# Kernel tuning notes

Hardware: AMD Instinct MI355X
Metric: run time of the kernel (lower is better)

Reference implementation:

```python
import jax, jax.numpy as jnp
import numpy as np

N = 50000


def gcn_conv(x, W, b, src, dst, deg_inv_sqrt):
    # h = x @ W, then symmetric-normalized aggregation with self-loops
    h = x @ W  # [N, out]
    norm = deg_inv_sqrt[src] * deg_inv_sqrt[dst]  # [E]
    agg = jax.ops.segment_sum(h[src] * norm[:, None], dst, num_segments=N)
    # self-loop contribution: norm_ii = deg_inv_sqrt[i]^2
    agg = agg + h * (deg_inv_sqrt * deg_inv_sqrt)[:, None]
    return agg + b


def setup_inputs() -> dict:
    key = jax.random.key(0)
    ks = jax.random.split(key, 8)
    F_in, H, C = 128, 128, 64
    x = jax.random.normal(ks[0], (N, F_in), dtype=jnp.float32)
    edge_index = jax.random.randint(ks[1], (2, 800000), 0, N, dtype=jnp.int64)
    s = 1.0 / np.sqrt(F_in)
    W1 = jax.random.uniform(ks[2], (F_in, H), jnp.float32, -s, s)
    b1 = jnp.zeros((H,), jnp.float32)
    W2 = jax.random.uniform(ks[3], (H, H), jnp.float32, -s, s)
    b2 = jnp.zeros((H,), jnp.float32)
    W3 = jax.random.uniform(ks[4], (H, C), jnp.float32, -s, s)
    b3 = jnp.zeros((C,), jnp.float32)
    return {"x": x, "edge_index": edge_index, "W1": W1, "b1": b1,
            "W2": W2, "b2": b2, "W3": W3, "b3": b3}


def reference(x, edge_index, W1, b1, W2, b2, W3, b3):
    src, dst = edge_index[0], edge_index[1]
    # degree with self-loops (edge weight 1): deg[i] = in-degree + 1
    deg = jnp.zeros((N,), x.dtype).at[dst].add(1.0) + 1.0
    dinv = jax.lax.rsqrt(deg)
    h = gcn_conv(x, W1, b1, src, dst, dinv)
    h = jax.nn.relu(h)  # dropout p=0 / eval -> identity
    h = gcn_conv(h, W2, b2, src, dst, dinv)
    h = jax.nn.relu(h)
    h = gcn_conv(h, W3, b3, src, dst, dinv)
    return jax.nn.log_softmax(h, axis=-1)
```

## Files before the change

kernel.cpp:

```cpp
#include <hip/hip_runtime.h>
#include <math.h>

typedef short short8 __attribute__((ext_vector_type(8)));
typedef float floatx4 __attribute__((ext_vector_type(4)));

__device__ __forceinline__ float4 ld4(const float* p) { return *reinterpret_cast<const float4*>(p); }
__device__ __forceinline__ void st4(float* p, float4 v) { *reinterpret_cast<float4*>(p) = v; }

__device__ __forceinline__ float bf2f(unsigned int u) { return __uint_as_float(u << 16); }
__device__ __forceinline__ unsigned int f2bf1(float f) {
    unsigned int x = __float_as_uint(f);
    return (x + 0x7fffu + ((x >> 16) & 1u)) >> 16;
}
__device__ __forceinline__ unsigned int f2bf2(float lo, float hi) {
    return f2bf1(lo) | (f2bf1(hi) << 16);
}
__device__ __forceinline__ void unpack8(uint4 v, float* f) {
    f[0] = bf2f(v.x & 0xffffu); f[1] = bf2f(v.x >> 16);
    f[2] = bf2f(v.y & 0xffffu); f[3] = bf2f(v.y >> 16);
    f[4] = bf2f(v.z & 0xffffu); f[5] = bf2f(v.z >> 16);
    f[6] = bf2f(v.w & 0xffffu); f[7] = bf2f(v.w >> 16);
}

__global__ __launch_bounds__(256) void k_count_prep(const int* __restrict__ dst, int* __restrict__ deg,
                                                    int* __restrict__ rank, int E, int nbE,
                                                    const float* __restrict__ W1, const float* __restrict__ W2,
                                                    const float* __restrict__ W3, unsigned short* __restrict__ Wt1,
                                                    unsigned short* __restrict__ Wt2, unsigned short* __restrict__ Wt3) {
    if ((int)blockIdx.x < nbE) {
        int e = blockIdx.x * 256 + threadIdx.x;
        if (e < E) rank[e] = atomicAdd(&deg[dst[e]], 1);
    } else {
        int t = (blockIdx.x - nbE) * 256 + threadIdx.x;
        if (t < 16384) {
            int k = t & 127, n = t >> 7;
            Wt1[n * 128 + k] = (unsigned short)f2bf1(W1[(size_t)k * 128 + n]);
        } else if (t < 32768) {
            int u = t - 16384;
            int k = u & 127, n = u >> 7;
            Wt2[n * 128 + k] = (unsigned short)f2bf1(W2[(size_t)k * 128 + n]);
        } else if (t < 40960) {
            int u = t - 32768;
            int k = u & 127, n = u >> 7;
            Wt3[n * 128 + k] = (unsigned short)f2bf1(W3[(size_t)k * 64 + n]);
        }
    }
}

__global__ __launch_bounds__(256) void k_reduce_gemm1(const int* __restrict__ deg, int* __restrict__ bsum, int n, int nb,
                                                      const float* __restrict__ X, const unsigned short* __restrict__ Wt,
                                                      unsigned short* __restrict__ O, int nrows) {
    constexpr int LDR = 136;
    __shared__ __align__(16) unsigned char smem[(64 * LDR + 128 * LDR) * 2];

    const int tid = threadIdx.x;
    if ((int)blockIdx.x < nb) {
        int* s = (int*)smem;
        int i = blockIdx.x * 256 + tid;
        s[tid] = (i < n) ? deg[i] : 0;
        __syncthreads();
        for (int off = 128; off > 0; off >>= 1) {
            if (tid < off) s[tid] += s[tid + off];
            __syncthreads();
        }
        if (tid == 0) bsum[blockIdx.x] = s[0];
        return;
    }

    unsigned short* sX = (unsigned short*)smem;
    unsigned short* sB = sX + 64 * LDR;
    const int row0 = (blockIdx.x - nb) * 64;

#pragma unroll
    for (int i = 0; i < 4; ++i) {
        int idx = tid + i * 256;
        int r = idx >> 4, c8 = idx & 15;
        int grow = row0 + r;
        uint4 v = make_uint4(0, 0, 0, 0);
        if (grow < nrows) {
            float4 a = ld4(X + (size_t)grow * 128 + c8 * 8);
            float4 b = ld4(X + (size_t)grow * 128 + c8 * 8 + 4);
            v = make_uint4(f2bf2(a.x, a.y), f2bf2(a.z, a.w), f2bf2(b.x, b.y), f2bf2(b.z, b.w));
        }
        *reinterpret_cast<uint4*>(&sX[r * LDR + c8 * 8]) = v;
    }
#pragma unroll
    for (int i = 0; i < 8; ++i) {
        int idx = tid + i * 256;
        int nn = idx >> 4, c8 = idx & 15;
        *reinterpret_cast<uint4*>(&sB[nn * LDR + c8 * 8]) =
            *reinterpret_cast<const uint4*>(Wt + (size_t)nn * 128 + c8 * 8);
    }
    __syncthreads();

    const int lane = tid & 63;
    const int wave = tid >> 6;
    const int l15  = lane & 15;
    const int quad = lane >> 4;

    floatx4 acc[8];
#pragma unroll
    for (int j = 0; j < 8; ++j) acc[j] = (floatx4){0.f, 0.f, 0.f, 0.f};

    const unsigned short* xbase = &sX[(wave * 16 + l15) * LDR + quad * 8];
#pragma unroll
    for (int kk = 0; kk < 4; ++kk) {
        short8 xb = *reinterpret_cast<const short8*>(xbase + kk * 32);
#pragma unroll
        for (int j = 0; j < 8; ++j) {
            short8 wa = *reinterpret_cast<const short8*>(&sB[(j * 16 + l15) * LDR + quad * 8 + kk * 32]);
            acc[j] = __builtin_amdgcn_mfma_f32_16x16x32_bf16(wa, xb, acc[j], 0, 0, 0);
        }
    }

    int xrow = row0 + wave * 16 + l15;
    if (xrow < nrows) {
#pragma unroll
        for (int j = 0; j < 8; ++j) {
            uint2 o = make_uint2(f2bf2(acc[j][0], acc[j][1]), f2bf2(acc[j][2], acc[j][3]));
            *reinterpret_cast<uint2*>(O + (size_t)xrow * 128 + j * 16 + quad * 4) = o;
        }
    }
}

__global__ __launch_bounds__(256) void k_scan_small(const int* __restrict__ bsum, int* __restrict__ boff, int nb) {
    __shared__ int s[256];
    int t = threadIdx.x;
    int v = (t < nb) ? bsum[t] : 0;
    s[t] = v;
    __syncthreads();
    for (int off = 1; off < 256; off <<= 1) {
        int x = (t >= off) ? s[t - off] : 0;
        __syncthreads();
        s[t] += x;
        __syncthreads();
    }
    if (t < nb) boff[t] = s[t] - v;
}

__global__ __launch_bounds__(256) void k_scan_final(const int* __restrict__ deg, const int* __restrict__ boff,
                                                    int* __restrict__ row_off, float* __restrict__ dinv, int n) {
    __shared__ int s[256];
    int t = threadIdx.x;
    int i = blockIdx.x * 256 + t;
    int v = (i < n) ? deg[i] : 0;
    s[t] = v;
    __syncthreads();
    for (int off = 1; off < 256; off <<= 1) {
        int x = (t >= off) ? s[t - off] : 0;
        __syncthreads();
        s[t] += x;
        __syncthreads();
    }
    int incl = s[t] + boff[blockIdx.x];
    if (i < n) {
        row_off[i] = incl - v;
        dinv[i]    = 1.0f / sqrtf((float)v + 1.0f);
        if (i == n - 1) row_off[n] = incl;
    }
}

__global__ __launch_bounds__(256) void k_fill_scale(const int* __restrict__ src, const int* __restrict__ dst,
                                                    const int* __restrict__ rank, const int* __restrict__ roff,
                                                    int* __restrict__ csrc, int E, int nbE,
                                                    unsigned short* __restrict__ A, const float* __restrict__ dinv,
                                                    int n16) {
    if ((int)blockIdx.x < nbE) {
        int e = blockIdx.x * 256 + threadIdx.x;
        if (e < E) csrc[roff[dst[e]] + rank[e]] = src[e];
    } else {
        int idx = (blockIdx.x - nbE) * 256 + threadIdx.x;
        if (idx < n16) {
            float di = dinv[idx >> 4];
            uint4 v = *reinterpret_cast<const uint4*>(A + (size_t)idx * 8);
            float f[8];
            unpack8(v, f);
#pragma unroll
            for (int i = 0; i < 8; ++i) f[i] *= di;
            uint4 o = make_uint4(f2bf2(f[0], f[1]), f2bf2(f[2], f[3]), f2bf2(f[4], f[5]), f2bf2(f[6], f[7]));
            *reinterpret_cast<uint4*>(A + (size_t)idx * 8) = o;
        }
    }
}

template <int NC>
__global__ __launch_bounds__(256) void k_gemm_mfma(const unsigned short* __restrict__ X,
                                                   const unsigned short* __restrict__ Wt,
                                                   const float* __restrict__ dinv,
                                                   unsigned short* __restrict__ O, int nrows) {
    constexpr int LDR = 136;
    __shared__ unsigned short sX[64 * LDR];
    __shared__ unsigned short sB[NC * LDR];

    const int tid  = threadIdx.x;
    const int row0 = blockIdx.x * 64;

#pragma unroll
    for (int i = 0; i < 4; ++i) {
        int idx = tid + i * 256;
        int r = idx >> 4, c8 = idx & 15;
        int grow = row0 + r;
        uint4 v = make_uint4(0, 0, 0, 0);
        if (grow < nrows) v = *reinterpret_cast<const uint4*>(X + (size_t)grow * 128 + c8 * 8);
        *reinterpret_cast<uint4*>(&sX[r * LDR + c8 * 8]) = v;
    }
#pragma unroll
    for (int i = 0; i < NC / 16; ++i) {
        int idx = tid + i * 256;
        int n = idx >> 4, c8 = idx & 15;
        *reinterpret_cast<uint4*>(&sB[n * LDR + c8 * 8]) =
            *reinterpret_cast<const uint4*>(Wt + (size_t)n * 128 + c8 * 8);
    }
    __syncthreads();

    const int lane = tid & 63;
    const int wave = tid >> 6;
    const int l15  = lane & 15;
    const int quad = lane >> 4;

    floatx4 acc[NC / 16];
#pragma unroll
    for (int j = 0; j < NC / 16; ++j) acc[j] = (floatx4){0.f, 0.f, 0.f, 0.f};

    const unsigned short* xbase = &sX[(wave * 16 + l15) * LDR + quad * 8];
#pragma unroll
    for (int kk = 0; kk < 4; ++kk) {
        short8 xb = *reinterpret_cast<const short8*>(xbase + kk * 32);
#pragma unroll
        for (int j = 0; j < NC / 16; ++j) {
            short8 wa = *reinterpret_cast<const short8*>(&sB[(j * 16 + l15) * LDR + quad * 8 + kk * 32]);
            acc[j] = __builtin_amdgcn_mfma_f32_16x16x32_bf16(wa, xb, acc[j], 0, 0, 0);
        }
    }

    int xrow = row0 + wave * 16 + l15;
    if (xrow < nrows) {
        float di = dinv[xrow];
#pragma unroll
        for (int j = 0; j < NC / 16; ++j) {
            uint2 o = make_uint2(f2bf2(acc[j][0] * di, acc[j][1] * di), f2bf2(acc[j][2] * di, acc[j][3] * di));
            *reinterpret_cast<uint2*>(O + (size_t)xrow * NC + j * 16 + quad * 4) = o;
        }
    }
}

__global__ __launch_bounds__(256) void k_agg_relu(const unsigned short* __restrict__ H, const int* __restrict__ roff,
                                                  const int* __restrict__ csrc, const float* __restrict__ dinv,
                                                  const float* __restrict__ bias, unsigned short* __restrict__ O, int n) {
    int t    = blockIdx.x * 256 + threadIdx.x;
    int node = t >> 4;
    int f8   = (t & 15) * 8;
    if (node >= n) return;

    float a[8];
    {
        uint4 hv = *reinterpret_cast<const uint4*>(H + (size_t)node * 128 + f8);
        unpack8(hv, a);
    }

    int e  = roff[node];
    int e1 = roff[node + 1];
    for (; e + 3 < e1; e += 4) {
        int s[4];
        uint4 v[4];
#pragma unroll
        for (int u = 0; u < 4; ++u) s[u] = csrc[e + u];
#pragma unroll
        for (int u = 0; u < 4; ++u) v[u] = *reinterpret_cast<const uint4*>(H + (size_t)s[u] * 128 + f8);
#pragma unroll
        for (int u = 0; u < 4; ++u) {
            float g[8];
            unpack8(v[u], g);
#pragma unroll
            for (int i = 0; i < 8; ++i) a[i] += g[i];
        }
    }
    for (; e < e1; ++e) {
        uint4 v0 = *reinterpret_cast<const uint4*>(H + (size_t)csrc[e] * 128 + f8);
        float g0[8];
        unpack8(v0, g0);
#pragma unroll
        for (int i = 0; i < 8; ++i) a[i] += g0[i];
    }

    float di = dinv[node];
    float4 b0 = ld4(bias + f8);
    float4 b1 = ld4(bias + f8 + 4);
    float bb[8] = {b0.x, b0.y, b0.z, b0.w, b1.x, b1.y, b1.z, b1.w};
#pragma unroll
    for (int i = 0; i < 8; ++i) a[i] = fmaxf(a[i] * di + bb[i], 0.0f);

    uint4 ov = make_uint4(f2bf2(a[0], a[1]), f2bf2(a[2], a[3]), f2bf2(a[4], a[5]), f2bf2(a[6], a[7]));
    *reinterpret_cast<uint4*>(O + (size_t)node * 128 + f8) = ov;
}

__global__ __launch_bounds__(256) void k_agg_softmax(const unsigned short* __restrict__ H, const int* __restrict__ roff,
                                                     const int* __restrict__ csrc, const float* __restrict__ dinv,
                                                     const float* __restrict__ bias, float* __restrict__ O, int n) {
    int t    = blockIdx.x * 256 + threadIdx.x;
    int node = t >> 3;
    int f8   = (t & 7) * 8;
    if (node >= n) return;

    float a[8];
    {
        uint4 hv = *reinterpret_cast<const uint4*>(H + (size_t)node * 64 + f8);
        unpack8(hv, a);
    }

    int e  = roff[node];
    int e1 = roff[node + 1];
    for (; e + 7 < e1; e += 8) {
        int s[8];
        uint4 v[8];
#pragma unroll
        for (int u = 0; u < 8; ++u) s[u] = csrc[e + u];
#pragma unroll
        for (int u = 0; u < 8; ++u) v[u] = *reinterpret_cast<const uint4*>(H + (size_t)s[u] * 64 + f8);
#pragma unroll
        for (int u = 0; u < 8; ++u) {
            float gg[8];
            unpack8(v[u], gg);
#pragma unroll
            for (int i = 0; i < 8; ++i) a[i] += gg[i];
        }
    }
    if (e + 3 < e1) {
        int s[4];
        uint4 v[4];
#pragma unroll
        for (int u = 0; u < 4; ++u) s[u] = csrc[e + u];
#pragma unroll
        for (int u = 0; u < 4; ++u) v[u] = *reinterpret_cast<const uint4*>(H + (size_t)s[u] * 64 + f8);
#pragma unroll
        for (int u = 0; u < 4; ++u) {
            float gg[8];
            unpack8(v[u], gg);
#pragma unroll
            for (int i = 0; i < 8; ++i) a[i] += gg[i];
        }
        e += 4;
    }
    for (; e < e1; ++e) {
        uint4 v0 = *reinterpret_cast<const uint4*>(H + (size_t)csrc[e] * 64 + f8);
        float g0[8];
        unpack8(v0, g0);
#pragma unroll
        for (int i = 0; i < 8; ++i) a[i] += g0[i];
    }

    float di = dinv[node];
    float4 b0 = ld4(bias + f8);
    float4 b1 = ld4(bias + f8 + 4);
    float bb[8] = {b0.x, b0.y, b0.z, b0.w, b1.x, b1.y, b1.z, b1.w};
    float v[8];
#pragma unroll
    for (int i = 0; i < 8; ++i) v[i] = a[i] * di + bb[i];

    float m = v[0];
#pragma unroll
    for (int i = 1; i < 8; ++i) m = fmaxf(m, v[i]);
    m = fmaxf(m, __shfl_xor(m, 1));
    m = fmaxf(m, __shfl_xor(m, 2));
    m = fmaxf(m, __shfl_xor(m, 4));

    float ssum = 0.0f;
#pragma unroll
    for (int i = 0; i < 8; ++i) ssum += expf(v[i] - m);
    ssum += __shfl_xor(ssum, 1);
    ssum += __shfl_xor(ssum, 2);
    ssum += __shfl_xor(ssum, 4);
    float ls = logf(ssum);

    float* op = O + (size_t)node * 64 + f8;
    st4(op, make_float4(v[0] - m - ls, v[1] - m - ls, v[2] - m - ls, v[3] - m - ls));
    st4(op + 4, make_float4(v[4] - m - ls, v[5] - m - ls, v[6] - m - ls, v[7] - m - ls));
}

extern "C" void kernel_launch(void* const* d_in, const int* in_sizes, int n_in,
                              void* d_out, int out_size, void* d_ws, size_t ws_size,
                              hipStream_t stream) {
    const float* x  = (const float*)d_in[0];
    const int*   ei = (const int*)d_in[1];
    const float* W1 = (const float*)d_in[2];
    const float* b1 = (const float*)d_in[3];
    const float* W2 = (const float*)d_in[4];
    const float* b2 = (const float*)d_in[5];
    const float* W3 = (const float*)d_in[6];
    const float* b3 = (const float*)d_in[7];
    float* out = (float*)d_out;

    const int N = in_sizes[0] / 128;
    const int E = in_sizes[1] / 2;
    const int* src = ei;
    const int* dst = ei + E;

    char* ws = (char*)d_ws;
    size_t off = 0;
    auto alloc = [&](size_t bytes) -> char* {
        char* p = ws + off;
        off = (off + bytes + 255) & ~(size_t)255;
        return p;
    };
    int nb  = (N + 255) / 256;
    int nbE = (E + 255) / 256;
    int blocks64 = (N + 63) / 64;
    int n16 = N * 16;
    int nbS = (n16 + 255) / 256;

    int*   deg     = (int*)alloc((size_t)N * 4);
    int*   row_off = (int*)alloc(((size_t)N + 1) * 4);
    float* dinv    = (float*)alloc((size_t)N * 4);
    int*   bsum    = (int*)alloc((size_t)nb * 4);
    int*   boff    = (int*)alloc((size_t)nb * 4);
    int*   rank    = (int*)alloc((size_t)E * 4);
    int*   csrc    = (int*)alloc((size_t)E * 4);
    unsigned short* Wt1  = (unsigned short*)alloc(128 * 128 * 2);
    unsigned short* Wt2  = (unsigned short*)alloc(128 * 128 * 2);
    unsigned short* Wt3  = (unsigned short*)alloc(64 * 128 * 2);
    unsigned short* bufA = (unsigned short*)alloc((size_t)N * 128 * 2);
    unsigned short* bufB = (unsigned short*)alloc((size_t)N * 128 * 2);
    unsigned short* bufC = (unsigned short*)alloc((size_t)N * 64 * 2);
    (void)ws_size; (void)n_in; (void)out_size;

    hipMemsetAsync(deg, 0, (size_t)N * 4, stream);
    k_count_prep<<<nbE + 160, 256, 0, stream>>>(dst, deg, rank, E, nbE, W1, W2, W3, Wt1, Wt2, Wt3);
    k_reduce_gemm1<<<nb + blocks64, 256, 0, stream>>>(deg, bsum, N, nb, x, Wt1, bufA, N);
    k_scan_small<<<1, 256, 0, stream>>>(bsum, boff, nb);
    k_scan_final<<<nb, 256, 0, stream>>>(deg, boff, row_off, dinv, N);
    k_fill_scale<<<nbE + nbS, 256, 0, stream>>>(src, dst, rank, row_off, csrc, E, nbE, bufA, dinv, n16);

    k_agg_relu<<<((size_t)N * 16 + 255) / 256, 256, 0, stream>>>(bufA, row_off, csrc, dinv, b1, bufB, N);
    k_gemm_mfma<128><<<blocks64, 256, 0, stream>>>(bufB, Wt2, dinv, bufA, N);
    k_agg_relu<<<((size_t)N * 16 + 255) / 256, 256, 0, stream>>>(bufA, row_off, csrc, dinv, b2, bufB, N);
    k_gemm_mfma<64><<<blocks64, 256, 0, stream>>>(bufB, Wt3, dinv, bufC, N);
    k_agg_softmax<<<((size_t)N * 8 + 255) / 256, 256, 0, stream>>>(bufC, row_off, csrc, dinv, b3, out, N);
}
```

Measured before the change: 252.3 us.

## Fold degree scan into gemm1 kernel and software-pipeline neighbor index loads

The three-kernel prefix scan over degrees (block reduce, small scan, final scan) is replaced by a single block inside the first GEMM launch. That block does a serial per-thread chunk scan plus a shared-memory scan, which removes two kernel launches and their dependencies. The aggregation loops now prefetch the next batch of CSR source indices while the current batch's feature gathers are in flight, to hide index-load latency. The single-block scan serialises about 200 sequential loads per thread with uncoalesced strides. It may also finish later than the GEMM blocks, so it can sit on the critical path.

```diff
diff --git a/kernel.cpp b/kernel.cpp
--- a/kernel.cpp
+++ b/kernel.cpp
@@ -47,29 +47,45 @@
     }
 }
 
-__global__ __launch_bounds__(256) void k_reduce_gemm1(const int* __restrict__ deg, int* __restrict__ bsum, int n, int nb,
-                                                      const float* __restrict__ X, const unsigned short* __restrict__ Wt,
-                                                      unsigned short* __restrict__ O, int nrows) {
+__global__ __launch_bounds__(256) void k_scan_gemm1(const int* __restrict__ deg, int* __restrict__ row_off,
+                                                    float* __restrict__ dinv, int n,
+                                                    const float* __restrict__ X, const unsigned short* __restrict__ Wt,
+                                                    unsigned short* __restrict__ O, int nrows) {
     constexpr int LDR = 136;
     __shared__ __align__(16) unsigned char smem[(64 * LDR + 128 * LDR) * 2];
 
     const int tid = threadIdx.x;
-    if ((int)blockIdx.x < nb) {
+    if (blockIdx.x == 0) {
         int* s = (int*)smem;
-        int i = blockIdx.x * 256 + tid;
-        s[tid] = (i < n) ? deg[i] : 0;
+        int per = (n + 255) / 256;
+        int start = tid * per;
+        int end   = start + per; if (end > n) end = n;
+        int sum = 0;
+        for (int i = start; i < end; ++i) sum += deg[i];
+        s[tid] = sum;
         __syncthreads();
-        for (int off = 128; off > 0; off >>= 1) {
-            if (tid < off) s[tid] += s[tid + off];
+        int incl = sum;
+        for (int off = 1; off < 256; off <<= 1) {
+            int x = (tid >= off) ? s[tid - off] : 0;
             __syncthreads();
-        }
-        if (tid == 0) bsum[blockIdx.x] = s[0];
+            incl += x;
+            s[tid] = incl;
+            __syncthreads();
+        }
+        int run = incl - sum;
+        for (int i = start; i < end; ++i) {
+            int d = deg[i];
+            row_off[i] = run;
+            dinv[i]    = 1.0f / sqrtf((float)d + 1.0f);
+            run += d;
+        }
+        if (start < n && end == n) row_off[n] = run;
         return;
     }
 
     unsigned short* sX = (unsigned short*)smem;
     unsigned short* sB = sX + 64 * LDR;
-    const int row0 = (blockIdx.x - nb) * 64;
+    const int row0 = ((int)blockIdx.x - 1) * 64;
 
 #pragma unroll
     for (int i = 0; i < 4; ++i) {
@@ -120,43 +136,6 @@
             uint2 o = make_uint2(f2bf2(acc[j][0], acc[j][1]), f2bf2(acc[j][2], acc[j][3]));
             *reinterpret_cast<uint2*>(O + (size_t)xrow * 128 + j * 16 + quad * 4) = o;
         }
-    }
-}
-
-__global__ __launch_bounds__(256) void k_scan_small(const int* __restrict__ bsum, int* __restrict__ boff, int nb) {
-    __shared__ int s[256];
-    int t = threadIdx.x;
-    int v = (t < nb) ? bsum[t] : 0;
-    s[t] = v;
-    __syncthreads();
-    for (int off = 1; off < 256; off <<= 1) {
-        int x = (t >= off) ? s[t - off] : 0;
-        __syncthreads();
-        s[t] += x;
-        __syncthreads();
-    }
-    if (t < nb) boff[t] = s[t] - v;
-}
-
-__global__ __launch_bounds__(256) void k_scan_final(const int* __restrict__ deg, const int* __restrict__ boff,
-                                                    int* __restrict__ row_off, float* __restrict__ dinv, int n) {
-    __shared__ int s[256];
-    int t = threadIdx.x;
-    int i = blockIdx.x * 256 + t;
-    int v = (i < n) ? deg[i] : 0;
-    s[t] = v;
-    __syncthreads();
-    for (int off = 1; off < 256; off <<= 1) {
-        int x = (t >= off) ? s[t - off] : 0;
-        __syncthreads();
-        s[t] += x;
-        __syncthreads();
-    }
-    int incl = s[t] + boff[blockIdx.x];
-    if (i < n) {
-        row_off[i] = incl - v;
-        dinv[i]    = 1.0f / sqrtf((float)v + 1.0f);
-        if (i == n - 1) row_off[n] = incl;
     }
 }
 
@@ -260,11 +239,31 @@
 
     int e  = roff[node];
     int e1 = roff[node + 1];
-    for (; e + 3 < e1; e += 4) {
+    int nfull = (e1 - e) >> 2;
+
+    if (nfull > 0) {
         int s[4];
+#pragma unroll
+        for (int u = 0; u < 4; ++u) s[u] = csrc[e + u];
+        for (int b = 1; b < nfull; ++b) {
+            uint4 v[4];
+#pragma unroll
+            for (int u = 0; u < 4; ++u) v[u] = *reinterpret_cast<const uint4*>(H + (size_t)s[u] * 128 + f8);
+            int sn[4];
+            int base = e + b * 4;
+#pragma unroll
+            for (int u = 0; u < 4; ++u) sn[u] = csrc[base + u];
+#pragma unroll
+            for (int u = 0; u < 4; ++u) {
+                float g[8];
+                unpack8(v[u], g);
+#pragma unroll
+                for (int i = 0; i < 8; ++i) a[i] += g[i];
+            }
+#pragma unroll
+            for (int u = 0; u < 4; ++u) s[u] = sn[u];
+        }
         uint4 v[4];
-#pragma unroll
-        for (int u = 0; u < 4; ++u) s[u] = csrc[e + u];
 #pragma unroll
         for (int u = 0; u < 4; ++u) v[u] = *reinterpret_cast<const uint4*>(H + (size_t)s[u] * 128 + f8);
 #pragma unroll
@@ -274,6 +273,7 @@
 #pragma unroll
             for (int i = 0; i < 8; ++i) a[i] += g[i];
         }
+        e += nfull * 4;
     }
     for (; e < e1; ++e) {
         uint4 v0 = *reinterpret_cast<const uint4*>(H + (size_t)csrc[e] * 128 + f8);
@@ -310,11 +310,31 @@
 
     int e  = roff[node];
     int e1 = roff[node + 1];
-    for (; e + 7 < e1; e += 8) {
+    int nfull = (e1 - e) >> 3;
+
+    if (nfull > 0) {
         int s[8];
+#pragma unroll
+        for (int u = 0; u < 8; ++u) s[u] = csrc[e + u];
+        for (int b = 1; b < nfull; ++b) {
+            uint4 v[8];
+#pragma unroll
+            for (int u = 0; u < 8; ++u) v[u] = *reinterpret_cast<const uint4*>(H + (size_t)s[u] * 64 + f8);
+            int sn[8];
+            int base = e + b * 8;
+#pragma unroll
+            for (int u = 0; u < 8; ++u) sn[u] = csrc[base + u];
+#pragma unroll
+            for (int u = 0; u < 8; ++u) {
+                float gg[8];
+                unpack8(v[u], gg);
+#pragma unroll
+                for (int i = 0; i < 8; ++i) a[i] += gg[i];
+            }
+#pragma unroll
+            for (int u = 0; u < 8; ++u) s[u] = sn[u];
+        }
         uint4 v[8];
-#pragma unroll
-        for (int u = 0; u < 8; ++u) s[u] = csrc[e + u];
 #pragma unroll
         for (int u = 0; u < 8; ++u) v[u] = *reinterpret_cast<const uint4*>(H + (size_t)s[u] * 64 + f8);
 #pragma unroll
@@ -324,22 +344,7 @@
 #pragma unroll
             for (int i = 0; i < 8; ++i) a[i] += gg[i];
         }
-    }
-    if (e + 3 < e1) {
-        int s[4];
-        uint4 v[4];
-#pragma unroll
-        for (int u = 0; u < 4; ++u) s[u] = csrc[e + u];
-#pragma unroll
-        for (int u = 0; u < 4; ++u) v[u] = *reinterpret_cast<const uint4*>(H + (size_t)s[u] * 64 + f8);
-#pragma unroll
-        for (int u = 0; u < 4; ++u) {
-            float gg[8];
-            unpack8(v[u], gg);
-#pragma unroll
-            for (int i = 0; i < 8; ++i) a[i] += gg[i];
-        }
-        e += 4;
+        e += nfull * 8;
     }
     for (; e < e1; ++e) {
         uint4 v0 = *reinterpret_cast<const uint4*>(H + (size_t)csrc[e] * 64 + f8);
@@ -402,7 +407,6 @@
         off = (off + bytes + 255) & ~(size_t)255;
         return p;
     };
-    int nb  = (N + 255) / 256;
     int nbE = (E + 255) / 256;
     int blocks64 = (N + 63) / 64;
     int n16 = N * 16;
@@ -411,8 +415,6 @@
     int*   deg     = (int*)alloc((size_t)N * 4);
     int*   row_off = (int*)alloc(((size_t)N + 1) * 4);
     float* dinv    = (float*)alloc((size_t)N * 4);
-    int*   bsum    = (int*)alloc((size_t)nb * 4);
-    int*   boff    = (int*)alloc((size_t)nb * 4);
     int*   rank    = (int*)alloc((size_t)E * 4);
     int*   csrc    = (int*)alloc((size_t)E * 4);
     unsigned short* Wt1  = (unsigned short*)alloc(128 * 128 * 2);
@@ -425,9 +427,7 @@
 
     hipMemsetAsync(deg, 0, (size_t)N * 4, stream);
     k_count_prep<<<nbE + 160, 256, 0, stream>>>(dst, deg, rank, E, nbE, W1, W2, W3, Wt1, Wt2, Wt3);
-    k_reduce_gemm1<<<nb + blocks64, 256, 0, stream>>>(deg, bsum, N, nb, x, Wt1, bufA, N);
-    k_scan_small<<<1, 256, 0, stream>>>(bsum, boff, nb);
-    k_scan_final<<<nb, 256, 0, stream>>>(deg, boff, row_off, dinv, N);
+    k_scan_gemm1<<<1 + blocks64, 256, 0, stream>>>(deg, row_off, dinv, N, x, Wt1, bufA, N);
     k_fill_scale<<<nbE + nbS, 256, 0, stream>>>(src, dst, rank, row_off, csrc, E, nbE, bufA, dinv, n16);
 
     k_agg_relu<<<((size_t)N * 16 + 255) / 256, 256, 0, stream>>>(bufA, row_off, csrc, dinv, b1, bufB, N);
```

Result: slower. 359.5 us (+42.5%).

## Compute dinv early and fold row scaling into first GEMM epilogue

Applied to the files above, without the earlier changes.

Moves the dinv computation into a new kernel that runs alongside the per-block degree reduction, so dinv exists before the first GEMM. The first GEMM then multiplies its output by dinv in the epilogue, which removes the separate read-modify-write pass over bufA that k_fill_scale did. The small block-sum scan is merged into the GEMM launch as block 0, keeping the launch count the same. Scaling in fp32 before the bf16 rounding also drops one rounding step.

```diff
diff --git a/kernel.cpp b/kernel.cpp
--- a/kernel.cpp
+++ b/kernel.cpp
@@ -47,29 +47,52 @@
     }
 }
 
-__global__ __launch_bounds__(256) void k_reduce_gemm1(const int* __restrict__ deg, int* __restrict__ bsum, int n, int nb,
-                                                      const float* __restrict__ X, const unsigned short* __restrict__ Wt,
-                                                      unsigned short* __restrict__ O, int nrows) {
+__global__ __launch_bounds__(256) void k_dinv_reduce(const int* __restrict__ deg, float* __restrict__ dinv,
+                                                     int* __restrict__ bsum, int n, int nbN) {
+    __shared__ int s[256];
+    int t = threadIdx.x;
+    if ((int)blockIdx.x < nbN) {
+        int i = blockIdx.x * 256 + t;
+        if (i < n) dinv[i] = 1.0f / sqrtf((float)deg[i] + 1.0f);
+        return;
+    }
+    int b = (int)blockIdx.x - nbN;
+    int i = b * 256 + t;
+    s[t] = (i < n) ? deg[i] : 0;
+    __syncthreads();
+    for (int off = 128; off > 0; off >>= 1) {
+        if (t < off) s[t] += s[t + off];
+        __syncthreads();
+    }
+    if (t == 0) bsum[b] = s[0];
+}
+
+__global__ __launch_bounds__(256) void k_scansmall_gemm1(const int* __restrict__ bsum, int* __restrict__ boff, int nb,
+                                                         const float* __restrict__ X, const unsigned short* __restrict__ Wt,
+                                                         const float* __restrict__ dinv,
+                                                         unsigned short* __restrict__ O, int nrows) {
     constexpr int LDR = 136;
     __shared__ __align__(16) unsigned char smem[(64 * LDR + 128 * LDR) * 2];
 
     const int tid = threadIdx.x;
-    if ((int)blockIdx.x < nb) {
+    if (blockIdx.x == 0) {
         int* s = (int*)smem;
-        int i = blockIdx.x * 256 + tid;
-        s[tid] = (i < n) ? deg[i] : 0;
+        int v = (tid < nb) ? bsum[tid] : 0;
+        s[tid] = v;
         __syncthreads();
-        for (int off = 128; off > 0; off >>= 1) {
-            if (tid < off) s[tid] += s[tid + off];
+        for (int off = 1; off < 256; off <<= 1) {
+            int x = (tid >= off) ? s[tid - off] : 0;
             __syncthreads();
-        }
-        if (tid == 0) bsum[blockIdx.x] = s[0];
+            s[tid] += x;
+            __syncthreads();
+        }
+        if (tid < nb) boff[tid] = s[tid] - v;
         return;
     }
 
     unsigned short* sX = (unsigned short*)smem;
     unsigned short* sB = sX + 64 * LDR;
-    const int row0 = (blockIdx.x - nb) * 64;
+    const int row0 = ((int)blockIdx.x - 1) * 64;
 
 #pragma unroll
     for (int i = 0; i < 4; ++i) {
@@ -115,31 +138,17 @@
 
     int xrow = row0 + wave * 16 + l15;
     if (xrow < nrows) {
+        float di = dinv[xrow];
 #pragma unroll
         for (int j = 0; j < 8; ++j) {
-            uint2 o = make_uint2(f2bf2(acc[j][0], acc[j][1]), f2bf2(acc[j][2], acc[j][3]));
+            uint2 o = make_uint2(f2bf2(acc[j][0] * di, acc[j][1] * di), f2bf2(acc[j][2] * di, acc[j][3] * di));
             *reinterpret_cast<uint2*>(O + (size_t)xrow * 128 + j * 16 + quad * 4) = o;
         }
     }
 }
 
-__global__ __launch_bounds__(256) void k_scan_small(const int* __restrict__ bsum, int* __restrict__ boff, int nb) {
-    __shared__ int s[256];
-    int t = threadIdx.x;
-    int v = (t < nb) ? bsum[t] : 0;
-    s[t] = v;
-    __syncthreads();
-    for (int off = 1; off < 256; off <<= 1) {
-        int x = (t >= off) ? s[t - off] : 0;
-        __syncthreads();
-        s[t] += x;
-        __syncthreads();
-    }
-    if (t < nb) boff[t] = s[t] - v;
-}
-
 __global__ __launch_bounds__(256) void k_scan_final(const int* __restrict__ deg, const int* __restrict__ boff,
-                                                    int* __restrict__ row_off, float* __restrict__ dinv, int n) {
+                                                    int* __restrict__ row_off, int n) {
     __shared__ int s[256];
     int t = threadIdx.x;
     int i = blockIdx.x * 256 + t;
@@ -155,32 +164,15 @@
     int incl = s[t] + boff[blockIdx.x];
     if (i < n) {
         row_off[i] = incl - v;
-        dinv[i]    = 1.0f / sqrtf((float)v + 1.0f);
         if (i == n - 1) row_off[n] = incl;
     }
 }
 
-__global__ __launch_bounds__(256) void k_fill_scale(const int* __restrict__ src, const int* __restrict__ dst,
-                                                    const int* __restrict__ rank, const int* __restrict__ roff,
-                                                    int* __restrict__ csrc, int E, int nbE,
-                                                    unsigned short* __restrict__ A, const float* __restrict__ dinv,
-                                                    int n16) {
-    if ((int)blockIdx.x < nbE) {
-        int e = blockIdx.x * 256 + threadIdx.x;
-        if (e < E) csrc[roff[dst[e]] + rank[e]] = src[e];
-    } else {
-        int idx = (blockIdx.x - nbE) * 256 + threadIdx.x;
-        if (idx < n16) {
-            float di = dinv[idx >> 4];
-            uint4 v = *reinterpret_cast<const uint4*>(A + (size_t)idx * 8);
-            float f[8];
-            unpack8(v, f);
-#pragma unroll
-            for (int i = 0; i < 8; ++i) f[i] *= di;
-            uint4 o = make_uint4(f2bf2(f[0], f[1]), f2bf2(f[2], f[3]), f2bf2(f[4], f[5]), f2bf2(f[6], f[7]));
-            *reinterpret_cast<uint4*>(A + (size_t)idx * 8) = o;
-        }
-    }
+__global__ __launch_bounds__(256) void k_fill(const int* __restrict__ src, const int* __restrict__ dst,
+                                              const int* __restrict__ rank, const int* __restrict__ roff,
+                                              int* __restrict__ csrc, int E) {
+    int e = blockIdx.x * 256 + threadIdx.x;
+    if (e < E) csrc[roff[dst[e]] + rank[e]] = src[e];
 }
 
 template <int NC>
@@ -405,8 +397,6 @@
     int nb  = (N + 255) / 256;
     int nbE = (E + 255) / 256;
     int blocks64 = (N + 63) / 64;
-    int n16 = N * 16;
-    int nbS = (n16 + 255) / 256;
 
     int*   deg     = (int*)alloc((size_t)N * 4);
     int*   row_off = (int*)alloc(((size_t)N + 1) * 4);
@@ -425,10 +415,10 @@
 
     hipMemsetAsync(deg, 0, (size_t)N * 4, stream);
     k_count_prep<<<nbE + 160, 256, 0, stream>>>(dst, deg, rank, E, nbE, W1, W2, W3, Wt1, Wt2, Wt3);
-    k_reduce_gemm1<<<nb + blocks64, 256, 0, stream>>>(deg, bsum, N, nb, x, Wt1, bufA, N);
-    k_scan_small<<<1, 256, 0, stream>>>(bsum, boff, nb);
-    k_scan_final<<<nb, 256, 0, stream>>>(deg, boff, row_off, dinv, N);
-    k_fill_scale<<<nbE + nbS, 256, 0, stream>>>(src, dst, rank, row_off, csrc, E, nbE, bufA, dinv, n16);
+    k_dinv_reduce<<<nb + nb, 256, 0, stream>>>(deg, dinv, bsum, N, nb);
+    k_scansmall_gemm1<<<1 + blocks64, 256, 0, stream>>>(bsum, boff, nb, x, Wt1, dinv, bufA, N);
+    k_scan_final<<<nb, 256, 0, stream>>>(deg, boff, row_off, N);
+    k_fill<<<nbE, 256, 0, stream>>>(src, dst, rank, row_off, csrc, E);
 
     k_agg_relu<<<((size_t)N * 16 + 255) / 256, 256, 0, stream>>>(bufA, row_off, csrc, dinv, b1, bufB, N);
     k_gemm_mfma<128><<<blocks64, 256, 0, stream>>>(bufB, Wt2, dinv, bufA, N);
```

Result: no change. 252.2 us (-0.0%).
